# Optimization experiments

Measured on AMD Instinct MI355X. Metric: run time of the kernel, lower is better.

Reference implementation:

```python
import jax, jax.numpy as jnp
import numpy as np

DIM, HEADS, WH, WW, NPROMPT, NW, BATCH = 384, 12, 7, 7, 5, 64, 32
N = WH * WW + NPROMPT  # 54


def _make_rel_index():
    ch, cw = np.meshgrid(np.arange(WH), np.arange(WW), indexing='ij')
    coords = np.stack([ch, cw]).reshape(2, -1)  # [2, 49]
    rel = coords[:, :, None] - coords[:, None, :]  # [2,49,49]
    rel = rel.transpose(1, 2, 0)
    rel[:, :, 0] += WH - 1
    rel[:, :, 1] += WW - 1
    rel[:, :, 0] *= 2 * WW - 1
    return rel.sum(-1).astype(np.int32)  # [49,49]


def setup_inputs() -> dict:
    key = jax.random.key(0)
    ks = jax.random.split(key, 7)
    B_ = BATCH * NW
    x = jax.random.normal(ks[0], (B_, N, DIM), jnp.float32)
    # 0/-inf style shifted-window mask; random floats exercise the same math
    mask = jnp.where(jax.random.uniform(ks[1], (NW, WH * WW, WH * WW)) > 0.8,
                     jnp.float32(-100.0), jnp.float32(0.0))
    qkv_w = 0.02 * jax.random.normal(ks[2], (3 * DIM, DIM), jnp.float32)
    qkv_b = 0.02 * jax.random.normal(ks[3], (3 * DIM,), jnp.float32)
    proj_w = 0.02 * jax.random.normal(ks[4], (DIM, DIM), jnp.float32)
    proj_b = 0.02 * jax.random.normal(ks[5], (DIM,), jnp.float32)
    rpb_table = 0.02 * jax.random.normal(ks[6], ((2 * WH - 1) * (2 * WW - 1), HEADS), jnp.float32)
    rel_index = jnp.asarray(_make_rel_index())
    return {"x": x, "mask": mask, "qkv_w": qkv_w, "qkv_b": qkv_b,
            "proj_w": proj_w, "proj_b": proj_b, "rpb_table": rpb_table,
            "rel_index": rel_index}


def reference(x, mask, qkv_w, qkv_b, proj_w, proj_b, rpb_table, rel_index):
    B_, n, C = x.shape
    hd = C // HEADS
    scale = hd ** -0.5
    qkv = (x @ qkv_w.T + qkv_b).reshape(B_, n, 3, HEADS, hd)
    qkv = jnp.moveaxis(qkv, 2, 0)  # [3, B_, n, H, hd]
    q, k, v = qkv[0], qkv[1], qkv[2]  # [B_, n, H, hd]
    attn = jnp.einsum('bnhd,bmhd->bhnm', q * scale, k)  # [B_, H, n, n]
    nw2 = WH * WW
    bias = rpb_table[rel_index.reshape(-1)].reshape(nw2, nw2, HEADS)
    bias = jnp.transpose(bias, (2, 0, 1))  # [H, 49, 49]
    bias = jnp.pad(bias, ((0, 0), (NPROMPT, 0), (NPROMPT, 0)))  # [H, n, n]
    attn = attn + bias[None]
    nW = mask.shape[0]
    mask_p = jnp.pad(mask, ((0, 0), (NPROMPT, 0), (NPROMPT, 0)))  # [nW, n, n]
    attn = attn.reshape(B_ // nW, nW, HEADS, n, n) + mask_p[None, :, None]
    attn = jax.nn.softmax(attn.reshape(B_, HEADS, n, n), axis=-1)
    out = jnp.einsum('bhnm,bmhd->bnhd', attn, v).reshape(B_, n, C)
    return out @ proj_w.T + proj_b
```

## Files before the change

### kernel.cpp

```cpp
#include <hip/hip_runtime.h>

#define DIM 384
#define NH 12
#define NT 54
#define NWIN 64
#define MTOT 110592
#define HS ((size_t)MTOT * 32)

typedef __attribute__((ext_vector_type(8))) short short8;
typedef __attribute__((ext_vector_type(4))) float f32x4;

__device__ __forceinline__ unsigned short f2bf(float f) {
  unsigned int u = __float_as_uint(f);
  u += 0x7fffu + ((u >> 16) & 1u);
  return (unsigned short)(u >> 16);
}
__device__ __forceinline__ float bf2f(unsigned short s) {
  return __uint_as_float((unsigned int)s << 16);
}
__device__ __forceinline__ unsigned int cvtpk(float a, float b) {
  unsigned int r;
  asm("v_cvt_pk_bf16_f32 %0, %1, %2" : "=v"(r) : "v"(a), "v"(b));
  return r;
}
__device__ __forceinline__ void gload16(const unsigned short* g,
                                        unsigned short* l) {
  __builtin_amdgcn_global_load_lds(
      (const __attribute__((address_space(1))) void*)g,
      (__attribute__((address_space(3))) void*)l, 16, 0, 0);
}

__global__ __launch_bounds__(256) void convert_x(
    const float* __restrict__ x, unsigned short* __restrict__ xb) {
  const size_t i8 = ((size_t)blockIdx.x * 256 + threadIdx.x) * 8;
  float4 fa = *(const float4*)&x[i8];
  float4 fb = *(const float4*)&x[i8 + 4];
  uint4 u;
  u.x = cvtpk(fa.x, fa.y);
  u.y = cvtpk(fa.z, fa.w);
  u.z = cvtpk(fb.x, fb.y);
  u.w = cvtpk(fb.z, fb.w);
  *(uint4*)&xb[i8] = u;
}

__global__ __launch_bounds__(256) void prep2_kernel(
    const float* __restrict__ qkv_w, const float* __restrict__ proj_w,
    const float* __restrict__ mask, const float* __restrict__ rpb,
    const int* __restrict__ rel,
    unsigned short* __restrict__ Wq, unsigned short* __restrict__ Wp,
    unsigned short* __restrict__ bmt) {
  int idx = blockIdx.x * 256 + threadIdx.x;
  if (idx < 1152 * 384) { Wq[idx] = f2bf(qkv_w[idx]); return; }
  idx -= 1152 * 384;
  if (idx < 384 * 384) { Wp[idx] = f2bf(proj_w[idx]); return; }
  idx -= 384 * 384;
  if (idx < NWIN * NH * 64 * 64) {
    int w = idx / (NH * 4096);
    int rem = idx - w * (NH * 4096);
    int h = rem >> 12, r = (rem >> 6) & 63, c = rem & 63;
    float v;
    if (r >= NT || c >= NT) v = -1e30f;
    else if (r >= 5 && c >= 5)
      v = rpb[rel[(r - 5) * 49 + (c - 5)] * NH + h] +
          mask[w * 2401 + (r - 5) * 49 + (c - 5)];
    else v = 0.0f;
    bmt[w * (NH * 4096) + (h << 12) + (c << 6) + r] = f2bf(v);
  }
}

__global__ __launch_bounds__(256) void qkv_gemm5(
    const unsigned short* __restrict__ xb, const unsigned short* __restrict__ Wq,
    const float* __restrict__ qkv_b,
    unsigned short* __restrict__ Qb, unsigned short* __restrict__ Kb,
    unsigned short* __restrict__ Vb) {
  __shared__ unsigned short As[128][64];
  __shared__ unsigned short Bs[128][64];
  const int s = blockIdx.x;
  const int xcd = s & 7, slot = s >> 3;
  const size_t m0 = (size_t)(xcd * 108 + slot / 9) * 128;
  const int n0 = (slot % 9) * 128;
  const int tid = threadIdx.x;
  const int wv = tid >> 6, ln = tid & 63, g = ln >> 4, lc = ln & 15;
  const int wr = (wv >> 1) * 64, wc = (wv & 1) * 64;
  const int l7 = lc & 7;
  const int lr8 = ln >> 3;
  const int sc8 = (((ln & 7) ^ lr8) & 7) * 8;

  f32x4 acc[4][4];
#pragma unroll
  for (int i = 0; i < 4; ++i)
#pragma unroll
    for (int j = 0; j < 4; ++j) acc[i][j] = (f32x4){0.f, 0.f, 0.f, 0.f};

#pragma unroll
  for (int kc = 0; kc < 6; ++kc) {
    const int k0 = kc * 64;
    if (kc) __syncthreads();
#pragma unroll
    for (int it = 0; it < 4; ++it) {
      const int r0 = wv * 32 + it * 8;
      const int r = r0 + lr8;
      gload16(&xb[(m0 + r) * 384 + k0 + sc8], &As[r0][0]);
      gload16(&Wq[(size_t)(n0 + r) * 384 + k0 + sc8], &Bs[r0][0]);
    }
    __syncthreads();
#pragma unroll
    for (int kk = 0; kk < 2; ++kk) {
      const int cix = (((kk * 4 + g) ^ l7)) * 8;
      short8 af[4], bfv[4];
#pragma unroll
      for (int ms = 0; ms < 4; ++ms)
        af[ms] = *(const short8*)&As[wr + ms * 16 + lc][cix];
#pragma unroll
      for (int ns = 0; ns < 4; ++ns)
        bfv[ns] = *(const short8*)&Bs[wc + ns * 16 + lc][cix];
#pragma unroll
      for (int ms = 0; ms < 4; ++ms)
#pragma unroll
        for (int ns = 0; ns < 4; ++ns)
          acc[ms][ns] = __builtin_amdgcn_mfma_f32_16x16x32_bf16(
              af[ms], bfv[ns], acc[ms][ns], 0, 0, 0);
    }
  }

  const int sel = n0 / 384;
  const float factor = (sel == 0) ? 0.17677669529663687f : 1.0f;
  unsigned short* outp = (sel == 0) ? Qb : (sel == 1 ? Kb : Vb);
#pragma unroll
  for (int ns = 0; ns < 4; ++ns) {
    const int n = n0 + wc + ns * 16 + lc;
    const int rl = n - sel * 384;
    const int h = rl >> 5, d = rl & 31;
    const float bias = qkv_b[n];
#pragma unroll
    for (int ms = 0; ms < 4; ++ms) {
      const size_t mrow = m0 + wr + ms * 16 + g * 4;
      const float v0 = (acc[ms][ns][0] + bias) * factor;
      const float v1 = (acc[ms][ns][1] + bias) * factor;
      const float v2 = (acc[ms][ns][2] + bias) * factor;
      const float v3 = (acc[ms][ns][3] + bias) * factor;
      const unsigned int u01 = cvtpk(v0, v1);
      const unsigned int u23 = cvtpk(v2, v3);
      unsigned short* p = &outp[(size_t)h * HS + mrow * 32 + d];
      p[0]  = (unsigned short)(u01 & 0xffffu);
      p[32] = (unsigned short)(u01 >> 16);
      p[64] = (unsigned short)(u23 & 0xffffu);
      p[96] = (unsigned short)(u23 >> 16);
    }
  }
}

__global__ __launch_bounds__(256) void attn5_kernel(
    unsigned short* __restrict__ Qb, const unsigned short* __restrict__ Kb,
    const unsigned short* __restrict__ Vb, const unsigned short* __restrict__ bmt) {
  __shared__ unsigned short Ps[2][NT][72];
  __shared__ unsigned short vT[2][32][72];
  const int s = blockIdx.x;
  const int xcd = s & 7, r3 = s >> 3;
  const int h = r3 % 12;
  const int t2 = r3 / 12;
  const int bp = t2 & 15;
  const int w = xcd * 8 + (t2 >> 4);
  const int tid = threadIdx.x;
  const int wv = tid >> 6, ln = tid & 63, g = ln >> 4, lc = ln & 15;
  const int m0 = wv * 16;
  const int arow = (m0 + lc < NT) ? (m0 + lc) : (NT - 1);
  unsigned short* Qh = Qb + (size_t)h * HS;
  const unsigned short* Kh = Kb + (size_t)h * HS;
  const unsigned short* Vh = Vb + (size_t)h * HS;
  const size_t base0 = (size_t)((bp * 2) * 64 + w) * NT;
  const size_t base1 = base0 + (size_t)64 * NT;

  for (int i = tid; i < 640; i += 256) {
    const int pi = (i >= 320) ? 1 : 0;
    const int j = i - pi * 320;
    const int d = j / 10, m = NT + (j - d * 10);
    vT[pi][d][m] = 0;
  }

  const int vr = tid >> 2, vc = (tid & 3) * 8;
  const unsigned short* bmh = &bmt[(size_t)(w * NH + h) << 12];
  const int row0 = m0 + g * 4;
  uint2 uu[4];
#pragma unroll
  for (int t = 0; t < 4; ++t)
    uu[t] = *(const uint2*)&bmh[((t * 16 + lc) << 6) + row0];

  short8 vv[2], a[2], kb[2][4];
#pragma unroll
  for (int pi = 0; pi < 2; ++pi) {
    const size_t base = pi ? base1 : base0;
    if (tid < 216)
      vv[pi] = *(const short8*)&Vh[(base + vr) * 32 + vc];
    a[pi] = *(const short8*)&Qh[(base + arow) * 32 + g * 8];
#pragma unroll
    for (int t = 0; t < 4; ++t) {
      const int col = t * 16 + lc;
      const int kr = (col < NT) ? col : (NT - 1);
      kb[pi][t] = *(const short8*)&Kh[(base + kr) * 32 + g * 8];
    }
  }

  f32x4 sac[2][4];
#pragma unroll
  for (int pi = 0; pi < 2; ++pi)
#pragma unroll
    for (int t = 0; t < 4; ++t) {
      f32x4 c0;
      c0[0] = bf2f((unsigned short)(uu[t].x & 0xffffu));
      c0[1] = bf2f((unsigned short)(uu[t].x >> 16));
      c0[2] = bf2f((unsigned short)(uu[t].y & 0xffffu));
      c0[3] = bf2f((unsigned short)(uu[t].y >> 16));
      sac[pi][t] = __builtin_amdgcn_mfma_f32_16x16x32_bf16(
          a[pi], kb[pi][t], c0, 0, 0, 0);
    }

  float rmax[2][4], rsum[2][4];
#pragma unroll
  for (int pi = 0; pi < 2; ++pi)
#pragma unroll
    for (int rr = 0; rr < 4; ++rr) rmax[pi][rr] = -3.0e38f;
#pragma unroll
  for (int pi = 0; pi < 2; ++pi)
#pragma unroll
    for (int t = 0; t < 4; ++t)
#pragma unroll
      for (int rr = 0; rr < 4; ++rr)
        rmax[pi][rr] = fmaxf(rmax[pi][rr], sac[pi][t][rr]);
#pragma unroll
  for (int pi = 0; pi < 2; ++pi)
#pragma unroll
    for (int rr = 0; rr < 4; ++rr)
#pragma unroll
      for (int off = 1; off < 16; off <<= 1)
        rmax[pi][rr] = fmaxf(rmax[pi][rr], __shfl_xor(rmax[pi][rr], off));
#pragma unroll
  for (int pi = 0; pi < 2; ++pi)
#pragma unroll
    for (int rr = 0; rr < 4; ++rr) rsum[pi][rr] = 0.f;
#pragma unroll
  for (int pi = 0; pi < 2; ++pi)
#pragma unroll
    for (int t = 0; t < 4; ++t)
#pragma unroll
      for (int rr = 0; rr < 4; ++rr) {
        float p = __expf(sac[pi][t][rr] - rmax[pi][rr]);
        sac[pi][t][rr] = p;
        rsum[pi][rr] += p;
      }
#pragma unroll
  for (int pi = 0; pi < 2; ++pi)
#pragma unroll
    for (int rr = 0; rr < 4; ++rr) {
#pragma unroll
      for (int off = 1; off < 16; off <<= 1)
        rsum[pi][rr] += __shfl_xor(rsum[pi][rr], off);
      rsum[pi][rr] = 1.0f / rsum[pi][rr];
    }
#pragma unroll
  for (int pi = 0; pi < 2; ++pi)
#pragma unroll
    for (int t = 0; t < 4; ++t) {
      const int col = t * 16 + lc;
      const unsigned int u01 =
          cvtpk(sac[pi][t][0] * rsum[pi][0], sac[pi][t][1] * rsum[pi][1]);
      const unsigned int u23 =
          cvtpk(sac[pi][t][2] * rsum[pi][2], sac[pi][t][3] * rsum[pi][3]);
      if (row0 < NT)     Ps[pi][row0][col]     = (unsigned short)(u01 & 0xffffu);
      if (row0 + 1 < NT) Ps[pi][row0 + 1][col] = (unsigned short)(u01 >> 16);
      if (row0 + 2 < NT) Ps[pi][row0 + 2][col] = (unsigned short)(u23 & 0xffffu);
      if (row0 + 3 < NT) Ps[pi][row0 + 3][col] = (unsigned short)(u23 >> 16);
    }
  if (tid < 216) {
#pragma unroll
    for (int pi = 0; pi < 2; ++pi)
#pragma unroll
      for (int j = 0; j < 8; ++j) vT[pi][vc + j][vr] = (unsigned short)vv[pi][j];
  }
  __syncthreads();
#pragma unroll
  for (int pi = 0; pi < 2; ++pi) {
    const size_t base = pi ? base1 : base0;
    f32x4 oac[2];
    oac[0] = (f32x4){0.f, 0.f, 0.f, 0.f};
    oac[1] = (f32x4){0.f, 0.f, 0.f, 0.f};
#pragma unroll
    for (int k2 = 0; k2 < 2; ++k2) {
      short8 pa = *(const short8*)&Ps[pi][arow][k2 * 32 + g * 8];
#pragma unroll
      for (int tn = 0; tn < 2; ++tn) {
        short8 vb = *(const short8*)&vT[pi][tn * 16 + lc][k2 * 32 + g * 8];
        oac[tn] = __builtin_amdgcn_mfma_f32_16x16x32_bf16(pa, vb, oac[tn], 0, 0, 0);
      }
    }
#pragma unroll
    for (int tn = 0; tn < 2; ++tn) {
      const int d = tn * 16 + lc;
      const unsigned int u01 = cvtpk(oac[tn][0], oac[tn][1]);
      const unsigned int u23 = cvtpk(oac[tn][2], oac[tn][3]);
      unsigned short* p = &Qh[(base + row0) * 32 + d];
      if (row0 < NT)     p[0]  = (unsigned short)(u01 & 0xffffu);
      if (row0 + 1 < NT) p[32] = (unsigned short)(u01 >> 16);
      if (row0 + 2 < NT) p[64] = (unsigned short)(u23 & 0xffffu);
      if (row0 + 3 < NT) p[96] = (unsigned short)(u23 >> 16);
    }
  }
}

__global__ __launch_bounds__(256) void proj_hmajor(
    const unsigned short* __restrict__ AO, const unsigned short* __restrict__ Wp,
    const float* __restrict__ proj_b, float* __restrict__ out) {
  __shared__ unsigned short As[128][72];
  __shared__ unsigned short Bs[128][72];
  const int s = blockIdx.x;
  const int xcd = s & 7, slot = s >> 3;
  const size_t m0 = (size_t)(xcd * 108 + slot / 3) * 128;
  const int n0 = (slot % 3) * 128;
  const int tid = threadIdx.x;
  const int wv = tid >> 6, ln = tid & 63, g = ln >> 4, lc = ln & 15;
  const int wr = (wv >> 1) * 64, wc = (wv & 1) * 64;
  f32x4 acc[4][4];
#pragma unroll
  for (int i = 0; i < 4; ++i)
#pragma unroll
    for (int j = 0; j < 4; ++j) acc[i][j] = (f32x4){0.f, 0.f, 0.f, 0.f};

  const int srow = tid >> 3, l8 = tid & 7;
  for (int kc = 0; kc < 6; ++kc) {
    const int k0 = kc * 64;
    const int kg = k0 + l8 * 8;
    const int hh = kg >> 5, dd = kg & 31;
#pragma unroll
    for (int it = 0; it < 4; ++it) {
      const int r = srow + it * 32;
      *(short8*)&As[r][l8 * 8] =
          *(const short8*)&AO[(size_t)hh * HS + (m0 + r) * 32 + dd];
      *(short8*)&Bs[r][l8 * 8] =
          *(const short8*)&Wp[(size_t)(n0 + r) * 384 + kg];
    }
    __syncthreads();
#pragma unroll
    for (int kk = 0; kk < 2; ++kk) {
      short8 af[4], bfv[4];
#pragma unroll
      for (int ms = 0; ms < 4; ++ms)
        af[ms] = *(const short8*)&As[wr + ms * 16 + lc][kk * 32 + g * 8];
#pragma unroll
      for (int ns = 0; ns < 4; ++ns)
        bfv[ns] = *(const short8*)&Bs[wc + ns * 16 + lc][kk * 32 + g * 8];
#pragma unroll
      for (int ms = 0; ms < 4; ++ms)
#pragma unroll
        for (int ns = 0; ns < 4; ++ns)
          acc[ms][ns] = __builtin_amdgcn_mfma_f32_16x16x32_bf16(
              af[ms], bfv[ns], acc[ms][ns], 0, 0, 0);
    }
    __syncthreads();
  }
#pragma unroll
  for (int ns = 0; ns < 4; ++ns) {
    const int n = n0 + wc + ns * 16 + lc;
    const float pb = proj_b[n];
#pragma unroll
    for (int ms = 0; ms < 4; ++ms)
#pragma unroll
      for (int rr = 0; rr < 4; ++rr) {
        const size_t m = m0 + wr + ms * 16 + g * 4 + rr;
        out[m * 384 + n] = acc[ms][ns][rr] + pb;
      }
  }
}

__global__ __launch_bounds__(256) void prep_kernel(
    const float* __restrict__ qkv_w, const float* __restrict__ proj_w,
    const float* __restrict__ mask, const float* __restrict__ rpb,
    const int* __restrict__ rel,
    unsigned short* __restrict__ Wq, unsigned short* __restrict__ Wp,
    float* __restrict__ bias_tab, float* __restrict__ maskp) {
  int idx = blockIdx.x * 256 + threadIdx.x;
  if (idx < 1152 * 384) { Wq[idx] = f2bf(qkv_w[idx]); return; }
  idx -= 1152 * 384;
  if (idx < 384 * 384) { Wp[idx] = f2bf(proj_w[idx]); return; }
  idx -= 384 * 384;
  if (idx < NH * 64 * 64) {
    int h = idx >> 12, r = (idx >> 6) & 63, c = idx & 63;
    float v;
    if (r >= NT || c >= NT) v = -1e30f;
    else if (r >= 5 && c >= 5) v = rpb[rel[(r - 5) * 49 + (c - 5)] * NH + h];
    else v = 0.0f;
    bias_tab[idx] = v;
    return;
  }
  idx -= NH * 64 * 64;
  if (idx < NWIN * 64 * 64) {
    int w = idx >> 12, r = (idx >> 6) & 63, c = idx & 63;
    float v = 0.0f;
    if (r >= 5 && r < NT && c >= 5 && c < NT)
      v = mask[w * 2401 + (r - 5) * 49 + (c - 5)];
    maskp[idx] = v;
  }
}

__global__ __launch_bounds__(256) void fused_attn(
    const float* __restrict__ x, const unsigned short* __restrict__ Wq,
    const float* __restrict__ qkv_b, const float* __restrict__ bias_tab,
    const float* __restrict__ maskp, unsigned short* __restrict__ AO) {
  __shared__ unsigned short xs[NT][392];
  __shared__ unsigned short qs[NT][40];
  __shared__ unsigned short ksm[NT][40];
  __shared__ unsigned short vT[32][72];
  __shared__ unsigned short Ps[NT][72];
  const int b = blockIdx.x;
  const int tid = threadIdx.x;
  const int wv = tid >> 6, ln = tid & 63;
  const int g = ln >> 4, lc = ln & 15;
  const int m0 = wv * 16;
  const int wi = b & 63;
  const float scale = 0.17677669529663687f;
  const float* xb = x + (size_t)b * (NT * DIM);
  for (int i = tid; i < NT * DIM / 4; i += 256) {
    float4 v = ((const float4*)xb)[i];
    int e = i * 4, r = e / DIM, c = e - r * DIM;
    unsigned short* p = &xs[r][c];
    p[0] = f2bf(v.x); p[1] = f2bf(v.y); p[2] = f2bf(v.z); p[3] = f2bf(v.w);
  }
  __syncthreads();
  const int arow = (m0 + lc < NT) ? (m0 + lc) : (NT - 1);
  for (int h = 0; h < NH; ++h) {
    f32x4 acc[6];
#pragma unroll
    for (int t = 0; t < 6; ++t) acc[t] = (f32x4){0.f, 0.f, 0.f, 0.f};
#pragma unroll 2
    for (int kk = 0; kk < 12; ++kk) {
      short8 a = *(const short8*)&xs[arow][kk * 32 + g * 8];
#pragma unroll
      for (int t = 0; t < 6; ++t) {
        const int sel = t >> 1;
        const int wrow = sel * 384 + h * 32 + (t & 1) * 16 + lc;
        short8 bfr = *(const short8*)&Wq[wrow * 384 + kk * 32 + g * 8];
        acc[t] = __builtin_amdgcn_mfma_f32_16x16x32_bf16(a, bfr, acc[t], 0, 0, 0);
      }
    }
#pragma unroll
    for (int t = 0; t < 6; ++t) {
      const int sel = t >> 1;
      const int d = (t & 1) * 16 + lc;
      const float bias = qkv_b[sel * 384 + h * 32 + d];
#pragma unroll
      for (int r = 0; r < 4; ++r) {
        const int m = m0 + g * 4 + r;
        float v = acc[t][r] + bias;
        if (sel == 2) vT[d][m] = f2bf(v);
        else if (m < NT) {
          if (sel == 0) qs[m][d] = f2bf(v * scale);
          else ksm[m][d] = f2bf(v);
        }
      }
    }
    __syncthreads();
    f32x4 sac[4];
    {
      short8 a = *(const short8*)&qs[arow][g * 8];
#pragma unroll
      for (int t = 0; t < 4; ++t) {
        const int kr = (t * 16 + lc < NT) ? (t * 16 + lc) : (NT - 1);
        short8 bfr = *(const short8*)&ksm[kr][g * 8];
        sac[t] = __builtin_amdgcn_mfma_f32_16x16x32_bf16(
            a, bfr, (f32x4){0.f, 0.f, 0.f, 0.f}, 0, 0, 0);
      }
    }
    const float* bt = bias_tab + h * 4096;
    const float* mp = maskp + wi * 4096;
    float sv[4][4];
    float rmax[4];
#pragma unroll
    for (int r = 0; r < 4; ++r) rmax[r] = -3.0e38f;
#pragma unroll
    for (int t = 0; t < 4; ++t) {
      const int col = t * 16 + lc;
#pragma unroll
      for (int r = 0; r < 4; ++r) {
        const int row = m0 + g * 4 + r;
        float s2 = sac[t][r] + bt[row * 64 + col] + mp[row * 64 + col];
        sv[t][r] = s2;
        rmax[r] = fmaxf(rmax[r], s2);
      }
    }
#pragma unroll
    for (int r = 0; r < 4; ++r)
#pragma unroll
      for (int off = 1; off < 16; off <<= 1)
        rmax[r] = fmaxf(rmax[r], __shfl_xor(rmax[r], off));
    float rsum[4] = {0.f, 0.f, 0.f, 0.f};
#pragma unroll
    for (int t = 0; t < 4; ++t)
#pragma unroll
      for (int r = 0; r < 4; ++r) {
        float p = __expf(sv[t][r] - rmax[r]);
        sv[t][r] = p;
        rsum[r] += p;
      }
#pragma unroll
    for (int r = 0; r < 4; ++r) {
#pragma unroll
      for (int off = 1; off < 16; off <<= 1)
        rsum[r] += __shfl_xor(rsum[r], off);
      rsum[r] = 1.0f / rsum[r];
    }
#pragma unroll
    for (int t = 0; t < 4; ++t) {
      const int col = t * 16 + lc;
#pragma unroll
      for (int r = 0; r < 4; ++r) {
        const int row = m0 + g * 4 + r;
        if (row < NT) Ps[row][col] = f2bf(sv[t][r] * rsum[r]);
      }
    }
    __syncthreads();
    f32x4 oac[2];
    oac[0] = (f32x4){0.f, 0.f, 0.f, 0.f};
    oac[1] = (f32x4){0.f, 0.f, 0.f, 0.f};
#pragma unroll
    for (int k2 = 0; k2 < 2; ++k2) {
      short8 a = *(const short8*)&Ps[arow][k2 * 32 + g * 8];
#pragma unroll
      for (int tn = 0; tn < 2; ++tn) {
        short8 bfr = *(const short8*)&vT[tn * 16 + lc][k2 * 32 + g * 8];
        oac[tn] = __builtin_amdgcn_mfma_f32_16x16x32_bf16(a, bfr, oac[tn], 0, 0, 0);
      }
    }
    unsigned short* aob = AO + (size_t)b * (NT * DIM) + h * 32;
#pragma unroll
    for (int tn = 0; tn < 2; ++tn) {
      const int d = tn * 16 + lc;
#pragma unroll
      for (int r = 0; r < 4; ++r) {
        const int m = m0 + g * 4 + r;
        if (m < NT) aob[m * DIM + d] = f2bf(oac[tn][r]);
      }
    }
    __syncthreads();
  }
}

__global__ __launch_bounds__(256) void proj_kernel(
    const unsigned short* __restrict__ AO, const unsigned short* __restrict__ Wp,
    const float* __restrict__ proj_b, float* __restrict__ out, int lda) {
  __shared__ unsigned short As[128][72];
  __shared__ unsigned short Bs[128][72];
  const int s = blockIdx.x;
  const int xcd = s & 7, slot = s >> 3;
  const size_t m0 = (size_t)(xcd * 108 + slot / 3) * 128;
  const int n0 = (slot % 3) * 128;
  const int tid = threadIdx.x;
  const int wv = tid >> 6, ln = tid & 63, g = ln >> 4, lc = ln & 15;
  const int wr = (wv >> 1) * 64, wc = (wv & 1) * 64;
  f32x4 acc[4][4];
#pragma unroll
  for (int i = 0; i < 4; ++i)
#pragma unroll
    for (int j = 0; j < 4; ++j) acc[i][j] = (f32x4){0.f, 0.f, 0.f, 0.f};

  const int srow = tid >> 3, l8 = tid & 7;
  for (int kc = 0; kc < 6; ++kc) {
    const int k0 = kc * 64;
#pragma unroll
    for (int it = 0; it < 4; ++it) {
      const int r = srow + it * 32;
      *(short8*)&As[r][l8 * 8] =
          *(const short8*)&AO[(m0 + r) * (size_t)lda + k0 + l8 * 8];
      *(short8*)&Bs[r][l8 * 8] =
          *(const short8*)&Wp[(size_t)(n0 + r) * 384 + k0 + l8 * 8];
    }
    __syncthreads();
#pragma unroll
    for (int kk = 0; kk < 2; ++kk) {
      short8 af[4], bfr[4];
#pragma unroll
      for (int ms = 0; ms < 4; ++ms)
        af[ms] = *(const short8*)&As[wr + ms * 16 + lc][kk * 32 + g * 8];
#pragma unroll
      for (int ns = 0; ns < 4; ++ns)
        bfr[ns] = *(const short8*)&Bs[wc + ns * 16 + lc][kk * 32 + g * 8];
#pragma unroll
      for (int ms = 0; ms < 4; ++ms)
#pragma unroll
        for (int ns = 0; ns < 4; ++ns)
          acc[ms][ns] = __builtin_amdgcn_mfma_f32_16x16x32_bf16(
              af[ms], bfr[ns], acc[ms][ns], 0, 0, 0);
    }
    __syncthreads();
  }
#pragma unroll
  for (int ns = 0; ns < 4; ++ns) {
    const int n = n0 + wc + ns * 16 + lc;
    const float pb = proj_b[n];
#pragma unroll
    for (int ms = 0; ms < 4; ++ms)
#pragma unroll
      for (int rr = 0; rr < 4; ++rr) {
        const size_t m = m0 + wr + ms * 16 + g * 4 + rr;
        out[m * 384 + n] = acc[ms][ns][rr] + pb;
      }
  }
}

extern "C" void kernel_launch(void* const* d_in, const int* in_sizes, int n_in,
                              void* d_out, int out_size, void* d_ws, size_t ws_size,
                              hipStream_t stream) {
  const float* x      = (const float*)d_in[0];
  const float* mask   = (const float*)d_in[1];
  const float* qkv_w  = (const float*)d_in[2];
  const float* qkv_b  = (const float*)d_in[3];
  const float* proj_w = (const float*)d_in[4];
  const float* proj_b = (const float*)d_in[5];
  const float* rpb    = (const float*)d_in[6];
  const int*   rel    = (const int*)d_in[7];
  float* out = (float*)d_out;

  const size_t QKV_ELEMS = (size_t)3 * NH * HS;
  const size_t WQ_ELEMS = 1152 * 384, WP_ELEMS = 384 * 384;
  const size_t BMT_ELEMS = (size_t)NWIN * NH * 4096;
  const size_t need = (QKV_ELEMS + WQ_ELEMS + WP_ELEMS + BMT_ELEMS) * 2;

  if (ws_size >= need) {
    unsigned short* Qb  = (unsigned short*)d_ws;
    unsigned short* Kb  = Qb + NH * HS;
    unsigned short* Vb  = Kb + NH * HS;
    unsigned short* Wq  = Vb + NH * HS;
    unsigned short* Wp  = Wq + WQ_ELEMS;
    unsigned short* bmt = Wp + WP_ELEMS;
    unsigned short* xb = (unsigned short*)d_out;

    convert_x<<<20736, 256, 0, stream>>>(x, xb);
    prep2_kernel<<<14592, 256, 0, stream>>>(qkv_w, proj_w, mask, rpb, rel,
                                            Wq, Wp, bmt);
    qkv_gemm5<<<7776, 256, 0, stream>>>(xb, Wq, qkv_b, Qb, Kb, Vb);
    attn5_kernel<<<12288, 256, 0, stream>>>(Qb, Kb, Vb, bmt);
    proj_hmajor<<<2592, 256, 0, stream>>>(Qb, Wp, proj_b, out);
  } else {
    unsigned short* Wq = (unsigned short*)d_ws;
    unsigned short* Wp = Wq + 442368;
    float* bias_tab = (float*)(Wp + 147456);
    float* maskp = bias_tab + 12 * 64 * 64;
    unsigned short* AO = (unsigned short*)(maskp + 64 * 64 * 64);
    prep_kernel<<<3520, 256, 0, stream>>>(qkv_w, proj_w, mask, rpb, rel,
                                          Wq, Wp, bias_tab, maskp);
    fused_attn<<<2048, 256, 0, stream>>>(x, Wq, qkv_b, bias_tab, maskp, AO);
    proj_kernel<<<2592, 256, 0, stream>>>(AO, Wp, proj_b, out, 384);
  }
}
```

Before: 398.1 us.

## Process four batch windows per attention block, overlapping second pair's softmax with first PV

The attention kernel now handles four batch instances per (window, head) block instead of two, halving the grid. It amortizes the mask/bias load across more windows and computes the second pair's QK and softmax while the first pair's PV results are held in registers, deferring all output stores to the end. This costs more registers and adds an extra barrier, which may reduce occupancy.

```diff
diff --git a/kernel.cpp b/kernel.cpp
--- a/kernel.cpp
+++ b/kernel.cpp
@@ -150,7 +150,7 @@
   }
 }
 
-__global__ __launch_bounds__(256) void attn5_kernel(
+__global__ __launch_bounds__(256) void attn6_kernel(
     unsigned short* __restrict__ Qb, const unsigned short* __restrict__ Kb,
     const unsigned short* __restrict__ Vb, const unsigned short* __restrict__ bmt) {
   __shared__ unsigned short Ps[2][NT][72];
@@ -159,8 +159,8 @@
   const int xcd = s & 7, r3 = s >> 3;
   const int h = r3 % 12;
   const int t2 = r3 / 12;
-  const int bp = t2 & 15;
-  const int w = xcd * 8 + (t2 >> 4);
+  const int bq = t2 & 7;
+  const int w = xcd * 8 + (t2 >> 3);
   const int tid = threadIdx.x;
   const int wv = tid >> 6, ln = tid & 63, g = ln >> 4, lc = ln & 15;
   const int m0 = wv * 16;
@@ -168,8 +168,8 @@
   unsigned short* Qh = Qb + (size_t)h * HS;
   const unsigned short* Kh = Kb + (size_t)h * HS;
   const unsigned short* Vh = Vb + (size_t)h * HS;
-  const size_t base0 = (size_t)((bp * 2) * 64 + w) * NT;
-  const size_t base1 = base0 + (size_t)64 * NT;
+  const int row0 = m0 + g * 4;
+  const int vr = tid >> 2, vc = (tid & 3) * 8;
 
   for (int i = tid; i < 640; i += 256) {
     const int pi = (i >= 320) ? 1 : 0;
@@ -178,94 +178,213 @@
     vT[pi][d][m] = 0;
   }
 
-  const int vr = tid >> 2, vc = (tid & 3) * 8;
   const unsigned short* bmh = &bmt[(size_t)(w * NH + h) << 12];
-  const int row0 = m0 + g * 4;
   uint2 uu[4];
 #pragma unroll
   for (int t = 0; t < 4; ++t)
     uu[t] = *(const uint2*)&bmh[((t * 16 + lc) << 6) + row0];
 
-  short8 vv[2], a[2], kb[2][4];
+  const size_t baseA0 = (size_t)((bq * 4 + 0) * 64 + w) * NT;
+  const size_t baseA1 = (size_t)((bq * 4 + 1) * 64 + w) * NT;
+  {
+    short8 vv[2], a[2], kb[2][4];
+#pragma unroll
+    for (int pi = 0; pi < 2; ++pi) {
+      const size_t base = pi ? baseA1 : baseA0;
+      if (tid < 216)
+        vv[pi] = *(const short8*)&Vh[(base + vr) * 32 + vc];
+      a[pi] = *(const short8*)&Qh[(base + arow) * 32 + g * 8];
+#pragma unroll
+      for (int t = 0; t < 4; ++t) {
+        const int col = t * 16 + lc;
+        const int kr = (col < NT) ? col : (NT - 1);
+        kb[pi][t] = *(const short8*)&Kh[(base + kr) * 32 + g * 8];
+      }
+    }
+    f32x4 sac[2][4];
+#pragma unroll
+    for (int pi = 0; pi < 2; ++pi)
+#pragma unroll
+      for (int t = 0; t < 4; ++t) {
+        f32x4 c0;
+        c0[0] = bf2f((unsigned short)(uu[t].x & 0xffffu));
+        c0[1] = bf2f((unsigned short)(uu[t].x >> 16));
+        c0[2] = bf2f((unsigned short)(uu[t].y & 0xffffu));
+        c0[3] = bf2f((unsigned short)(uu[t].y >> 16));
+        sac[pi][t] = __builtin_amdgcn_mfma_f32_16x16x32_bf16(
+            a[pi], kb[pi][t], c0, 0, 0, 0);
+      }
+    float rmax[2][4], rsum[2][4];
+#pragma unroll
+    for (int pi = 0; pi < 2; ++pi)
+#pragma unroll
+      for (int rr = 0; rr < 4; ++rr) rmax[pi][rr] = -3.0e38f;
+#pragma unroll
+    for (int pi = 0; pi < 2; ++pi)
+#pragma unroll
+      for (int t = 0; t < 4; ++t)
+#pragma unroll
+        for (int rr = 0; rr < 4; ++rr)
+          rmax[pi][rr] = fmaxf(rmax[pi][rr], sac[pi][t][rr]);
+#pragma unroll
+    for (int pi = 0; pi < 2; ++pi)
+#pragma unroll
+      for (int rr = 0; rr < 4; ++rr)
+#pragma unroll
+        for (int off = 1; off < 16; off <<= 1)
+          rmax[pi][rr] = fmaxf(rmax[pi][rr], __shfl_xor(rmax[pi][rr], off));
+#pragma unroll
+    for (int pi = 0; pi < 2; ++pi)
+#pragma unroll
+      for (int rr = 0; rr < 4; ++rr) rsum[pi][rr] = 0.f;
+#pragma unroll
+    for (int pi = 0; pi < 2; ++pi)
+#pragma unroll
+      for (int t = 0; t < 4; ++t)
+#pragma unroll
+        for (int rr = 0; rr < 4; ++rr) {
+          float p = __expf(sac[pi][t][rr] - rmax[pi][rr]);
+          sac[pi][t][rr] = p;
+          rsum[pi][rr] += p;
+        }
+#pragma unroll
+    for (int pi = 0; pi < 2; ++pi)
+#pragma unroll
+      for (int rr = 0; rr < 4; ++rr) {
+#pragma unroll
+        for (int off = 1; off < 16; off <<= 1)
+          rsum[pi][rr] += __shfl_xor(rsum[pi][rr], off);
+        rsum[pi][rr] = 1.0f / rsum[pi][rr];
+      }
+#pragma unroll
+    for (int pi = 0; pi < 2; ++pi)
+#pragma unroll
+      for (int t = 0; t < 4; ++t) {
+        const int col = t * 16 + lc;
+        const unsigned int u01 =
+            cvtpk(sac[pi][t][0] * rsum[pi][0], sac[pi][t][1] * rsum[pi][1]);
+        const unsigned int u23 =
+            cvtpk(sac[pi][t][2] * rsum[pi][2], sac[pi][t][3] * rsum[pi][3]);
+        if (row0 < NT)     Ps[pi][row0][col]     = (unsigned short)(u01 & 0xffffu);
+        if (row0 + 1 < NT) Ps[pi][row0 + 1][col] = (unsigned short)(u01 >> 16);
+        if (row0 + 2 < NT) Ps[pi][row0 + 2][col] = (unsigned short)(u23 & 0xffffu);
+        if (row0 + 3 < NT) Ps[pi][row0 + 3][col] = (unsigned short)(u23 >> 16);
+      }
+    if (tid < 216) {
+#pragma unroll
+      for (int pi = 0; pi < 2; ++pi)
+#pragma unroll
+        for (int j = 0; j < 8; ++j)
+          vT[pi][vc + j][vr] = (unsigned short)vv[pi][j];
+    }
+  }
+  __syncthreads();
+  f32x4 oacA[2][2];
 #pragma unroll
   for (int pi = 0; pi < 2; ++pi) {
-    const size_t base = pi ? base1 : base0;
-    if (tid < 216)
-      vv[pi] = *(const short8*)&Vh[(base + vr) * 32 + vc];
-    a[pi] = *(const short8*)&Qh[(base + arow) * 32 + g * 8];
+    oacA[pi][0] = (f32x4){0.f, 0.f, 0.f, 0.f};
+    oacA[pi][1] = (f32x4){0.f, 0.f, 0.f, 0.f};
+#pragma unroll
+    for (int k2 = 0; k2 < 2; ++k2) {
+      short8 pa = *(const short8*)&Ps[pi][arow][k2 * 32 + g * 8];
+#pragma unroll
+      for (int tn = 0; tn < 2; ++tn) {
+        short8 vb = *(const short8*)&vT[pi][tn * 16 + lc][k2 * 32 + g * 8];
+        oacA[pi][tn] = __builtin_amdgcn_mfma_f32_16x16x32_bf16(
+            pa, vb, oacA[pi][tn], 0, 0, 0);
+      }
+    }
+  }
+
+  const size_t baseB0 = (size_t)((bq * 4 + 2) * 64 + w) * NT;
+  const size_t baseB1 = (size_t)((bq * 4 + 3) * 64 + w) * NT;
+  short8 vvB[2];
+  f32x4 sacB[2][4];
+  {
+    short8 a[2], kb[2][4];
+#pragma unroll
+    for (int pi = 0; pi < 2; ++pi) {
+      const size_t base = pi ? baseB1 : baseB0;
+      if (tid < 216)
+        vvB[pi] = *(const short8*)&Vh[(base + vr) * 32 + vc];
+      a[pi] = *(const short8*)&Qh[(base + arow) * 32 + g * 8];
+#pragma unroll
+      for (int t = 0; t < 4; ++t) {
+        const int col = t * 16 + lc;
+        const int kr = (col < NT) ? col : (NT - 1);
+        kb[pi][t] = *(const short8*)&Kh[(base + kr) * 32 + g * 8];
+      }
+    }
+#pragma unroll
+    for (int pi = 0; pi < 2; ++pi)
+#pragma unroll
+      for (int t = 0; t < 4; ++t) {
+        f32x4 c0;
+        c0[0] = bf2f((unsigned short)(uu[t].x & 0xffffu));
+        c0[1] = bf2f((unsigned short)(uu[t].x >> 16));
+        c0[2] = bf2f((unsigned short)(uu[t].y & 0xffffu));
+        c0[3] = bf2f((unsigned short)(uu[t].y >> 16));
+        sacB[pi][t] = __builtin_amdgcn_mfma_f32_16x16x32_bf16(
+            a[pi], kb[pi][t], c0, 0, 0, 0);
+      }
+    float rmax[2][4], rsum[2][4];
+#pragma unroll
+    for (int pi = 0; pi < 2; ++pi)
+#pragma unroll
+      for (int rr = 0; rr < 4; ++rr) rmax[pi][rr] = -3.0e38f;
+#pragma unroll
+    for (int pi = 0; pi < 2; ++pi)
+#pragma unroll
+      for (int t = 0; t < 4; ++t)
+#pragma unroll
+        for (int rr = 0; rr < 4; ++rr)
+          rmax[pi][rr] = fmaxf(rmax[pi][rr], sacB[pi][t][rr]);
+#pragma unroll
+    for (int pi = 0; pi < 2; ++pi)
+#pragma unroll
+      for (int rr = 0; rr < 4; ++rr)
+#pragma unroll
+        for (int off = 1; off < 16; off <<= 1)
+          rmax[pi][rr] = fmaxf(rmax[pi][rr], __shfl_xor(rmax[pi][rr], off));
+#pragma unroll
+    for (int pi = 0; pi < 2; ++pi)
+#pragma unroll
+      for (int rr = 0; rr < 4; ++rr) rsum[pi][rr] = 0.f;
+#pragma unroll
+    for (int pi = 0; pi < 2; ++pi)
+#pragma unroll
+      for (int t = 0; t < 4; ++t)
+#pragma unroll
+        for (int rr = 0; rr < 4; ++rr) {
+          float p = __expf(sacB[pi][t][rr] - rmax[pi][rr]);
+          sacB[pi][t][rr] = p;
+          rsum[pi][rr] += p;
+        }
+#pragma unroll
+    for (int pi = 0; pi < 2; ++pi)
+#pragma unroll
+      for (int rr = 0; rr < 4; ++rr) {
+#pragma unroll
+        for (int off = 1; off < 16; off <<= 1)
+          rsum[pi][rr] += __shfl_xor(rsum[pi][rr], off);
+        rsum[pi][rr] = 1.0f / rsum[pi][rr];
+      }
+#pragma unroll
+    for (int pi = 0; pi < 2; ++pi)
+#pragma unroll
+      for (int t = 0; t < 4; ++t)
+#pragma unroll
+        for (int rr = 0; rr < 4; ++rr)
+          sacB[pi][t][rr] *= rsum[pi][rr];
+  }
+  __syncthreads();
+#pragma unroll
+  for (int pi = 0; pi < 2; ++pi)
 #pragma unroll
     for (int t = 0; t < 4; ++t) {
       const int col = t * 16 + lc;
-      const int kr = (col < NT) ? col : (NT - 1);
-      kb[pi][t] = *(const short8*)&Kh[(base + kr) * 32 + g * 8];
-    }
-  }
-
-  f32x4 sac[2][4];
-#pragma unroll
-  for (int pi = 0; pi < 2; ++pi)
-#pragma unroll
-    for (int t = 0; t < 4; ++t) {
-      f32x4 c0;
-      c0[0] = bf2f((unsigned short)(uu[t].x & 0xffffu));
-      c0[1] = bf2f((unsigned short)(uu[t].x >> 16));
-      c0[2] = bf2f((unsigned short)(uu[t].y & 0xffffu));
-      c0[3] = bf2f((unsigned short)(uu[t].y >> 16));
-      sac[pi][t] = __builtin_amdgcn_mfma_f32_16x16x32_bf16(
-          a[pi], kb[pi][t], c0, 0, 0, 0);
-    }
-
-  float rmax[2][4], rsum[2][4];
-#pragma unroll
-  for (int pi = 0; pi < 2; ++pi)
-#pragma unroll
-    for (int rr = 0; rr < 4; ++rr) rmax[pi][rr] = -3.0e38f;
-#pragma unroll
-  for (int pi = 0; pi < 2; ++pi)
-#pragma unroll
-    for (int t = 0; t < 4; ++t)
-#pragma unroll
-      for (int rr = 0; rr < 4; ++rr)
-        rmax[pi][rr] = fmaxf(rmax[pi][rr], sac[pi][t][rr]);
-#pragma unroll
-  for (int pi = 0; pi < 2; ++pi)
-#pragma unroll
-    for (int rr = 0; rr < 4; ++rr)
-#pragma unroll
-      for (int off = 1; off < 16; off <<= 1)
-        rmax[pi][rr] = fmaxf(rmax[pi][rr], __shfl_xor(rmax[pi][rr], off));
-#pragma unroll
-  for (int pi = 0; pi < 2; ++pi)
-#pragma unroll
-    for (int rr = 0; rr < 4; ++rr) rsum[pi][rr] = 0.f;
-#pragma unroll
-  for (int pi = 0; pi < 2; ++pi)
-#pragma unroll
-    for (int t = 0; t < 4; ++t)
-#pragma unroll
-      for (int rr = 0; rr < 4; ++rr) {
-        float p = __expf(sac[pi][t][rr] - rmax[pi][rr]);
-        sac[pi][t][rr] = p;
-        rsum[pi][rr] += p;
-      }
-#pragma unroll
-  for (int pi = 0; pi < 2; ++pi)
-#pragma unroll
-    for (int rr = 0; rr < 4; ++rr) {
-#pragma unroll
-      for (int off = 1; off < 16; off <<= 1)
-        rsum[pi][rr] += __shfl_xor(rsum[pi][rr], off);
-      rsum[pi][rr] = 1.0f / rsum[pi][rr];
-    }
-#pragma unroll
-  for (int pi = 0; pi < 2; ++pi)
-#pragma unroll
-    for (int t = 0; t < 4; ++t) {
-      const int col = t * 16 + lc;
-      const unsigned int u01 =
-          cvtpk(sac[pi][t][0] * rsum[pi][0], sac[pi][t][1] * rsum[pi][1]);
-      const unsigned int u23 =
-          cvtpk(sac[pi][t][2] * rsum[pi][2], sac[pi][t][3] * rsum[pi][3]);
+      const unsigned int u01 = cvtpk(sacB[pi][t][0], sacB[pi][t][1]);
+      const unsigned int u23 = cvtpk(sacB[pi][t][2], sacB[pi][t][3]);
       if (row0 < NT)     Ps[pi][row0][col]     = (unsigned short)(u01 & 0xffffu);
       if (row0 + 1 < NT) Ps[pi][row0 + 1][col] = (unsigned short)(u01 >> 16);
       if (row0 + 2 < NT) Ps[pi][row0 + 2][col] = (unsigned short)(u23 & 0xffffu);
@@ -275,30 +394,43 @@
 #pragma unroll
     for (int pi = 0; pi < 2; ++pi)
 #pragma unroll
-      for (int j = 0; j < 8; ++j) vT[pi][vc + j][vr] = (unsigned short)vv[pi][j];
+      for (int j = 0; j < 8; ++j)
+        vT[pi][vc + j][vr] = (unsigned short)vvB[pi][j];
   }
   __syncthreads();
+  f32x4 oacB[2][2];
 #pragma unroll
   for (int pi = 0; pi < 2; ++pi) {
-    const size_t base = pi ? base1 : base0;
-    f32x4 oac[2];
-    oac[0] = (f32x4){0.f, 0.f, 0.f, 0.f};
-    oac[1] = (f32x4){0.f, 0.f, 0.f, 0.f};
+    oacB[pi][0] = (f32x4){0.f, 0.f, 0.f, 0.f};
+    oacB[pi][1] = (f32x4){0.f, 0.f, 0.f, 0.f};
 #pragma unroll
     for (int k2 = 0; k2 < 2; ++k2) {
       short8 pa = *(const short8*)&Ps[pi][arow][k2 * 32 + g * 8];
 #pragma unroll
       for (int tn = 0; tn < 2; ++tn) {
         short8 vb = *(const short8*)&vT[pi][tn * 16 + lc][k2 * 32 + g * 8];
-        oac[tn] = __builtin_amdgcn_mfma_f32_16x16x32_bf16(pa, vb, oac[tn], 0, 0, 0);
-      }
-    }
+        oacB[pi][tn] = __builtin_amdgcn_mfma_f32_16x16x32_bf16(
+            pa, vb, oacB[pi][tn], 0, 0, 0);
+      }
+    }
+  }
+#pragma unroll
+  for (int pi = 0; pi < 2; ++pi) {
+    const size_t baseA = pi ? baseA1 : baseA0;
+    const size_t baseB = pi ? baseB1 : baseB0;
 #pragma unroll
     for (int tn = 0; tn < 2; ++tn) {
       const int d = tn * 16 + lc;
-      const unsigned int u01 = cvtpk(oac[tn][0], oac[tn][1]);
-      const unsigned int u23 = cvtpk(oac[tn][2], oac[tn][3]);
-      unsigned short* p = &Qh[(base + row0) * 32 + d];
+      unsigned int u01 = cvtpk(oacA[pi][tn][0], oacA[pi][tn][1]);
+      unsigned int u23 = cvtpk(oacA[pi][tn][2], oacA[pi][tn][3]);
+      unsigned short* p = &Qh[(baseA + row0) * 32 + d];
+      if (row0 < NT)     p[0]  = (unsigned short)(u01 & 0xffffu);
+      if (row0 + 1 < NT) p[32] = (unsigned short)(u01 >> 16);
+      if (row0 + 2 < NT) p[64] = (unsigned short)(u23 & 0xffffu);
+      if (row0 + 3 < NT) p[96] = (unsigned short)(u23 >> 16);
+      u01 = cvtpk(oacB[pi][tn][0], oacB[pi][tn][1]);
+      u23 = cvtpk(oacB[pi][tn][2], oacB[pi][tn][3]);
+      p = &Qh[(baseB + row0) * 32 + d];
       if (row0 < NT)     p[0]  = (unsigned short)(u01 & 0xffffu);
       if (row0 + 1 < NT) p[32] = (unsigned short)(u01 >> 16);
       if (row0 + 2 < NT) p[64] = (unsigned short)(u23 & 0xffffu);
@@ -636,7 +768,7 @@
     prep2_kernel<<<14592, 256, 0, stream>>>(qkv_w, proj_w, mask, rpb, rel,
                                             Wq, Wp, bmt);
     qkv_gemm5<<<7776, 256, 0, stream>>>(xb, Wq, qkv_b, Qb, Kb, Vb);
-    attn5_kernel<<<12288, 256, 0, stream>>>(Qb, Kb, Vb, bmt);
+    attn6_kernel<<<6144, 256, 0, stream>>>(Qb, Kb, Vb, bmt);
     proj_hmajor<<<2592, 256, 0, stream>>>(Qb, Wp, proj_b, out);
   } else {
     unsigned short* Wq = (unsigned short*)d_ws;
```

Result: no change. 399.9 us (+0.4%).
